# Performance work log

Measured on AMD Instinct MI355X. Metric: run time of the kernel, lower is better.

Reference implementation:

```python
import jax, jax.numpy as jnp
import numpy as np

SCALING = 2.5
OFFSET = 0.0
TIME_LENGTH = 10.0
DT = 0.1
CUTOFF = TIME_LENGTH  # cutoff=None -> time_length
TIME_STEPS = int(TIME_LENGTH // DT) + 1  # == 100 (float floor: 10.0//0.1 == 99.0)
CENTERS = np.array([-1.75, -1.25, -0.75, -0.25, 0.25, 0.75, 1.25, 1.75], dtype=np.float32)


def setup_inputs() -> dict:
    key = jax.random.key(0)
    k1, = jax.random.split(key, 1)
    trace = jax.random.normal(k1, (1024, 128), dtype=jnp.float32)
    center = jnp.asarray(CENTERS)
    return {"trace": trace, "center": center, "dummy1": 0, "dummy2": 0}


def reference(trace, center, dummy1, dummy2):
    B = trace.shape[0]
    # times: [B, F*C] latency per (feature, center) pair
    times = SCALING * jnp.abs(trace[..., None] - center).reshape(B, -1)
    times = jnp.where((times < 0) | (times > CUTOFF), TIME_LENGTH + DT, times)
    times = times + OFFSET
    bins = (times / DT + 1).astype(jnp.int32)  # trunc == floor for positive values
    mask = bins < TIME_STEPS
    N = times.shape[1]
    bi = jnp.broadcast_to(jnp.arange(B)[:, None], (B, N))
    ni = jnp.broadcast_to(jnp.arange(N)[None, :], (B, N))
    bins_c = jnp.clip(bins, 0, TIME_STEPS - 1)
    vals = mask.astype(jnp.int32)
    # masked scatter-add into pre-zeroed dense spike tensor (COO to_dense sums dups)
    spikes = jnp.zeros((TIME_STEPS, B, N), dtype=jnp.int32).at[bins_c, bi, ni].add(vals)
    return spikes
```

## Files before the change

kernel.cpp:

```cpp
#include <hip/hip_runtime.h>
#include <hip/hip_bf16.h>


#define BB 1024
#define FF 128
#define NN 1024
#define TT 100
#define GROUPS_PER_PLANE ((BB * NN) / 4)
#define WINDOW 2048
#define WINS (GROUPS_PER_PLANE / WINDOW)
#define PCH 10
#define PCHUNKS (TT / PCH)

typedef int iv4 __attribute__((ext_vector_type(4)));

__global__ __launch_bounds__(256) void arnold_bins_kernel(
        const float* __restrict__ trace,
        const float* __restrict__ center,
        uchar4* __restrict__ bins) {
    const int b   = blockIdx.x;
    const int tid = threadIdx.x;
    const int n0  = tid << 2;
    const int f   = n0 >> 3;
    const int c0  = n0 & 7;

    const float x = trace[b * FF + f];

    unsigned char v[4];
#pragma unroll
    for (int i = 0; i < 4; ++i) {
        float tms = 2.5f * fabsf(x - center[c0 + i]);
        unsigned bb = (tms > 10.0f) ? 255u : (unsigned)(tms / 0.1f + 1.0f);
        v[i] = (unsigned char)bb;
    }
    bins[(b << 8) + tid] = make_uchar4(v[0], v[1], v[2], v[3]);
}

__global__ __launch_bounds__(256) void arnold_stream_kernel(
        const uchar4* __restrict__ bins,
        iv4* __restrict__ out) {
    __shared__ uchar4 lb[WINDOW];
    const int w   = blockIdx.x;
    const int pc  = blockIdx.y;
    const int tid = threadIdx.x;

    const uchar4* bw = bins + w * WINDOW;
#pragma unroll
    for (int i = 0; i < WINDOW / 256; ++i) lb[i * 256 + tid] = bw[i * 256 + tid];
    __syncthreads();

    const int t0 = pc * PCH;
    iv4* base = out + (size_t)w * WINDOW;
    for (int tt = 0; tt < PCH; ++tt) {
        const int t = t0 + tt;
        iv4* op = base + (size_t)t * GROUPS_PER_PLANE;
#pragma unroll
        for (int i = 0; i < WINDOW / 256; ++i) {
            const int idx = i * 256 + tid;
            const uchar4 c = lb[idx];
            iv4 v;
            v.x = (c.x == t) ? 1 : 0;
            v.y = (c.y == t) ? 1 : 0;
            v.z = (c.z == t) ? 1 : 0;
            v.w = (c.w == t) ? 1 : 0;
            __builtin_nontemporal_store(v, &op[idx]);
        }
    }
}

extern "C" void kernel_launch(void* const* d_in, const int* in_sizes, int n_in,
                              void* d_out, int out_size, void* d_ws, size_t ws_size,
                              hipStream_t stream) {
    const float* trace  = (const float*)d_in[0];
    const float* center = (const float*)d_in[1];
    uchar4* bins = (uchar4*)d_ws;
    iv4* out = (iv4*)d_out;

    arnold_bins_kernel<<<BB, 256, 0, stream>>>(trace, center, bins);
    dim3 grid(WINS, PCHUNKS);
    arnold_stream_kernel<<<grid, 256, 0, stream>>>(bins, out);
}
```

Before: 418.6 us.

## Replace windowed LDS stream kernel with grid-stride linear sweep over output

The output write kernel no longer stages a window of bins in shared memory and loops over time chunks. Instead 512 persistent blocks sweep the whole output linearly with a grid stride, reading each bin group from global memory (cached in L2) for every time plane. This removes the LDS staging and __syncthreads and makes the stores contiguous across the grid, at the cost of rereading the 1 MB bins array from cache once per plane and running fewer blocks.

```diff
diff --git a/kernel.cpp b/kernel.cpp
--- a/kernel.cpp
+++ b/kernel.cpp
@@ -1,16 +1,14 @@
 #include <hip/hip_runtime.h>
-#include <hip/hip_bf16.h>
 
 
 #define BB 1024
 #define FF 128
-#define NN 1024
 #define TT 100
-#define GROUPS_PER_PLANE ((BB * NN) / 4)
-#define WINDOW 2048
-#define WINS (GROUPS_PER_PLANE / WINDOW)
-#define PCH 10
-#define PCHUNKS (TT / PCH)
+#define PLANE_GROUPS ((BB * 1024) / 4)
+#define TOTAL_GROUPS (TT * PLANE_GROUPS)
+#define SWEEP_BLOCKS 512
+#define SWEEP_STRIDE (SWEEP_BLOCKS * 256)
+#define SWEEP_ITERS (TOTAL_GROUPS / SWEEP_STRIDE)
 
 typedef int iv4 __attribute__((ext_vector_type(4)));
 
@@ -36,35 +34,21 @@
     bins[(b << 8) + tid] = make_uchar4(v[0], v[1], v[2], v[3]);
 }
 
-__global__ __launch_bounds__(256) void arnold_stream_kernel(
+__global__ __launch_bounds__(256) void arnold_sweep_kernel(
         const uchar4* __restrict__ bins,
         iv4* __restrict__ out) {
-    __shared__ uchar4 lb[WINDOW];
-    const int w   = blockIdx.x;
-    const int pc  = blockIdx.y;
-    const int tid = threadIdx.x;
-
-    const uchar4* bw = bins + w * WINDOW;
-#pragma unroll
-    for (int i = 0; i < WINDOW / 256; ++i) lb[i * 256 + tid] = bw[i * 256 + tid];
-    __syncthreads();
-
-    const int t0 = pc * PCH;
-    iv4* base = out + (size_t)w * WINDOW;
-    for (int tt = 0; tt < PCH; ++tt) {
-        const int t = t0 + tt;
-        iv4* op = base + (size_t)t * GROUPS_PER_PLANE;
-#pragma unroll
-        for (int i = 0; i < WINDOW / 256; ++i) {
-            const int idx = i * 256 + tid;
-            const uchar4 c = lb[idx];
-            iv4 v;
-            v.x = (c.x == t) ? 1 : 0;
-            v.y = (c.y == t) ? 1 : 0;
-            v.z = (c.z == t) ? 1 : 0;
-            v.w = (c.w == t) ? 1 : 0;
-            __builtin_nontemporal_store(v, &op[idx]);
-        }
+    unsigned g = blockIdx.x * 256u + threadIdx.x;
+#pragma unroll 4
+    for (int k = 0; k < SWEEP_ITERS; ++k) {
+        const unsigned t = g >> 18;
+        const uchar4 c = bins[g & (PLANE_GROUPS - 1)];
+        iv4 v;
+        v.x = (c.x == t) ? 1 : 0;
+        v.y = (c.y == t) ? 1 : 0;
+        v.z = (c.z == t) ? 1 : 0;
+        v.w = (c.w == t) ? 1 : 0;
+        __builtin_nontemporal_store(v, out + g);
+        g += SWEEP_STRIDE;
     }
 }
 
@@ -77,6 +61,5 @@
     iv4* out = (iv4*)d_out;
 
     arnold_bins_kernel<<<BB, 256, 0, stream>>>(trace, center, bins);
-    dim3 grid(WINS, PCHUNKS);
-    arnold_stream_kernel<<<grid, 256, 0, stream>>>(bins, out);
+    arnold_sweep_kernel<<<SWEEP_BLOCKS, 256, 0, stream>>>(bins, out);
 }
```

New measurement: 411.5 us. About the same (-1.7%).
